# Kernel tuning notes

Measured on AMD Instinct MI355X. Metric: run time of the kernel, lower is better.

The kernel has to match this reference:

```python
import jax, jax.numpy as jnp
import numpy as np

N = 100_000      # nodes
M = 200_000      # hyperedges
E = 1_000_000    # incidence pairs
D_IN = 64
HEADS, D_OUT = 8, 16   # linear out = 8*16 = 128


def setup_inputs() -> dict:
    key = jax.random.key(0)
    k = jax.random.split(key, 7)
    X = jax.random.normal(k[0], (N, D_IN), dtype=jnp.float32)
    vertex = jax.random.randint(k[1], (E,), 0, N, dtype=jnp.int32)
    edges = jax.random.randint(k[2], (E,), 0, M, dtype=jnp.int32)
    dege = jax.random.uniform(k[3], (M, 1), dtype=jnp.float32)
    degv = jax.random.uniform(k[4], (N, 1), dtype=jnp.float32)
    W = jax.random.normal(k[5], (D_IN, HEADS * D_OUT), dtype=jnp.float32) / np.sqrt(D_IN)
    b = jax.random.normal(k[6], (HEADS * D_OUT,), dtype=jnp.float32) * 0.01
    return {"X": X, "vertex": vertex, "edges": edges, "dege": dege, "degv": degv, "W": W, "b": b}


def reference(X, vertex, edges, dege, degv, W, b):
    n_nodes = X.shape[0]
    n_edges = dege.shape[0]
    # vertex -> hyperedge aggregation (first_aggregate = 'mean')
    Xve = X[vertex]                                               # [E, D]
    sums = jax.ops.segment_sum(Xve, edges, num_segments=n_edges)  # [M, D]
    counts = jax.ops.segment_sum(jnp.ones((edges.shape[0],), X.dtype), edges, num_segments=n_edges)
    Xe = sums / jnp.maximum(counts, 1.0)[:, None]                 # empty edges -> 0
    Xe = Xe * dege
    # hyperedge -> vertex aggregation (sum)
    Xev = Xe[edges]                                               # [E, D]
    Xv = jax.ops.segment_sum(Xev, vertex, num_segments=n_nodes)   # [N, D]
    Xv = Xv * degv
    # normalize_l2: row norm is computed on a DETACHED tensor in torch
    rownorm = jnp.linalg.norm(jax.lax.stop_gradient(Xv), axis=1, keepdims=True)
    scale = jnp.where(rownorm > 0, 1.0 / rownorm, 0.0)
    Xn = Xv * scale
    return Xn @ W + b
```

## Files before the change

kernel.cpp:

```cpp
#include <hip/hip_runtime.h>


#define DIN 64
#define DOUT 128
#define CH 4096
#define BSHIFT 10
#define PAYBITS 18
#define PAYMASK ((1u << PAYBITS) - 1u)

typedef float f32x4 __attribute__((ext_vector_type(4)));
typedef short bf16x8 __attribute__((ext_vector_type(8)));

__device__ __forceinline__ unsigned short f2b(float f) {
  unsigned u = __float_as_uint(f);
  u = u + 0x7fffu + ((u >> 16) & 1u);
  return (unsigned short)(u >> 16);
}
__device__ __forceinline__ float b2f(unsigned s) {
  return __uint_as_float(s << 16);
}

__global__ __launch_bounds__(256) void p1_hist(
    const int* __restrict__ vertex, const int* __restrict__ edges,
    int* __restrict__ G, int E, int BKE, int BK, int NCH) {
  __shared__ int h[512];
  for (int i = threadIdx.x; i < BK; i += 256) h[i] = 0;
  __syncthreads();
  int c = blockIdx.x;
  int s = c * CH, e_ = min(E, s + CH);
  for (int i = s + threadIdx.x; i < e_; i += 256) {
    atomicAdd(&h[edges[i] >> BSHIFT], 1);
    atomicAdd(&h[BKE + (vertex[i] >> BSHIFT)], 1);
  }
  __syncthreads();
  for (int b = threadIdx.x; b < BK; b += 256) G[(size_t)b * NCH + c] = h[b];
}

__global__ __launch_bounds__(256) void p1b_rowscan(
    int* __restrict__ G, int* __restrict__ rowTot, int NCH) {
  int b = blockIdx.x;
  int* row = G + (size_t)b * NCH;
  __shared__ int wsum[4];
  __shared__ int carry;
  if (threadIdx.x == 0) carry = 0;
  __syncthreads();
  for (int base = 0; base < NCH; base += 256) {
    int i = base + threadIdx.x;
    int v = (i < NCH) ? row[i] : 0;
    int lane = threadIdx.x & 63, wid = threadIdx.x >> 6;
    int inc = v;
    #pragma unroll
    for (int o = 1; o < 64; o <<= 1) {
      int t = __shfl_up(inc, o);
      if (lane >= o) inc += t;
    }
    if (lane == 63) wsum[wid] = inc;
    __syncthreads();
    int woff = carry;
    for (int w = 0; w < wid; ++w) woff += wsum[w];
    int excl = woff + inc - v;
    if (i < NCH) row[i] = excl;
    __syncthreads();
    if (threadIdx.x == 0) carry += wsum[0] + wsum[1] + wsum[2] + wsum[3];
    __syncthreads();
  }
  if (threadIdx.x == 0) rowTot[b] = carry;
}

__global__ void p1c_scan(const int* __restrict__ rowTot,
                         int* __restrict__ bucketBase, int BK) {
  if (threadIdx.x == 0 && blockIdx.x == 0) {
    int s = 0;
    for (int b = 0; b < BK; ++b) { bucketBase[b] = s; s += rowTot[b]; }
    bucketBase[BK] = s;
  }
}

__global__ __launch_bounds__(256) void p2_scatter(
    const int* __restrict__ vertex, const int* __restrict__ edges,
    const int* __restrict__ G, const int* __restrict__ bucketBase,
    unsigned* __restrict__ temp, int E, int BKE, int BK, int NCH) {
  __shared__ int curs[512];
  int c = blockIdx.x;
  for (int b = threadIdx.x; b < BK; b += 256)
    curs[b] = bucketBase[b] + G[(size_t)b * NCH + c];
  __syncthreads();
  int s = c * CH, e_ = min(E, s + CH);
  for (int i = s + threadIdx.x; i < e_; i += 256) {
    int e = edges[i], v = vertex[i];
    int pE = atomicAdd(&curs[e >> BSHIFT], 1);
    temp[pE] = ((unsigned)(e & 1023) << PAYBITS) | (unsigned)v;
    int pV = atomicAdd(&curs[BKE + (v >> BSHIFT)], 1);
    temp[pV] = ((unsigned)(v & 1023) << PAYBITS) | (unsigned)e;
  }
}

__global__ __launch_bounds__(256) void p3_sort(
    const unsigned* __restrict__ temp, const int* __restrict__ bucketBase,
    int* __restrict__ off, int* __restrict__ perm, int BKE, int M, int N) {
  __shared__ int hist[1024];
  __shared__ int pos[1024];
  __shared__ int wsum[4];
  int g = blockIdx.x;
  bool isE = g < BKE;
  int gg = isE ? g : g - BKE;
  int keyBase = gg << BSHIFT;
  int cap = isE ? M : N;
  int offBase = (isE ? 0 : M) + keyBase;
  int fineCount = min(1024, cap - keyBase);
  int pairBase = bucketBase[g], pairEnd = bucketBase[g + 1];
  int cnt = pairEnd - pairBase;

  for (int i = threadIdx.x; i < 1024; i += 256) hist[i] = 0;
  __syncthreads();
  for (int i = threadIdx.x; i < cnt; i += 256)
    atomicAdd(&hist[temp[pairBase + i] >> PAYBITS], 1);
  __syncthreads();

  int t4 = threadIdx.x * 4;
  int a0 = hist[t4], a1 = hist[t4 + 1], a2 = hist[t4 + 2], a3 = hist[t4 + 3];
  int tsum = a0 + a1 + a2 + a3;
  int lane = threadIdx.x & 63, wid = threadIdx.x >> 6;
  int inc = tsum;
  #pragma unroll
  for (int o = 1; o < 64; o <<= 1) {
    int t = __shfl_up(inc, o);
    if (lane >= o) inc += t;
  }
  if (lane == 63) wsum[wid] = inc;
  __syncthreads();
  int woff = 0;
  for (int w = 0; w < wid; ++w) woff += wsum[w];
  int excl = woff + inc - tsum;
  pos[t4] = excl; pos[t4 + 1] = excl + a0;
  pos[t4 + 2] = excl + a0 + a1; pos[t4 + 3] = excl + a0 + a1 + a2;
  __syncthreads();

  for (int f = threadIdx.x; f < fineCount; f += 256)
    off[offBase + f] = pairBase + pos[f] + hist[f];
  for (int f = threadIdx.x; f < 1024; f += 256) pos[f] += pairBase;
  __syncthreads();

  for (int i = threadIdx.x; i < cnt; i += 256) {
    unsigned p = temp[pairBase + i];
    int q = atomicAdd(&pos[p >> PAYBITS], 1);
    perm[q] = (int)(p & PAYMASK);
  }
}


__global__ __launch_bounds__(256) void k_xcast(
    const float* __restrict__ X, unsigned short* __restrict__ Xb, int total4) {
  int i = blockIdx.x * 256 + threadIdx.x;
  if (i >= total4) return;
  float4 a = ((const float4*)X)[i];
  ushort4 r;
  r.x = f2b(a.x); r.y = f2b(a.y); r.z = f2b(a.z); r.w = f2b(a.w);
  ((ushort4*)Xb)[i] = r;
}

__global__ __launch_bounds__(256) void k_edge(
    const unsigned short* __restrict__ Xb, const int* __restrict__ off,
    const int* __restrict__ perm, const float* __restrict__ dege,
    unsigned short* __restrict__ Xe, int M) {
  long long gid = (long long)blockIdx.x * 256 + threadIdx.x;
  int wv = (int)(gid >> 6);
  int lane = threadIdx.x & 63;
  int g = lane >> 4, li = lane & 15;
  int e = wv * 4 + g;
  bool valid = e < M;
  int start = 0, end = 0;
  if (valid) { start = e ? off[e - 1] : 0; end = off[e]; }
  int deg = end - start;
  int myidx = (valid && li < deg) ? perm[start + li] : 0;
  int jmax = min(deg, 16);
  int jw = jmax;
  jw = max(jw, __shfl_xor(jw, 16));
  jw = max(jw, __shfl_xor(jw, 32));
  const uint2* X2 = (const uint2*)Xb;
  float4 acc = make_float4(0.f, 0.f, 0.f, 0.f);
  #pragma unroll 4
  for (int j = 0; j < jw; ++j) {
    int v0 = __shfl(myidx, (g << 4) + j);
    if (j < jmax) {
      uint2 a = X2[(size_t)v0 * 16 + li];
      acc.x += b2f(a.x & 0xffffu); acc.y += b2f(a.x >> 16);
      acc.z += b2f(a.y & 0xffffu); acc.w += b2f(a.y >> 16);
    }
  }
  for (int j = 16; j < deg; ++j) {
    int v0 = perm[start + j];
    uint2 a = X2[(size_t)v0 * 16 + li];
    acc.x += b2f(a.x & 0xffffu); acc.y += b2f(a.x >> 16);
    acc.z += b2f(a.y & 0xffffu); acc.w += b2f(a.y >> 16);
  }
  if (valid) {
    float s = dege[e] / fmaxf((float)deg, 1.0f);
    ushort4 r;
    r.x = f2b(acc.x * s); r.y = f2b(acc.y * s);
    r.z = f2b(acc.z * s); r.w = f2b(acc.w * s);
    ((ushort4*)Xe)[(size_t)e * 16 + li] = r;
  }
}

__global__ __launch_bounds__(256) void k_nodeagg(
    const unsigned short* __restrict__ Xe, const int* __restrict__ off,
    const int* __restrict__ perm, const float* __restrict__ degv,
    unsigned short* __restrict__ xn, int N, int M) {
  long long gid = (long long)blockIdx.x * 256 + threadIdx.x;
  int wv = (int)(gid >> 6);
  int lane = threadIdx.x & 63;
  int g = lane >> 4, li = lane & 15;
  int node = wv * 4 + g;
  bool valid = node < N;
  int start = 0, end = 0;
  if (valid) { start = off[M + node - 1]; end = off[M + node]; }
  int deg = end - start;
  int myidx = (valid && li < deg) ? perm[start + li] : 0;
  int jmax = min(deg, 16);
  int jw = jmax;
  jw = max(jw, __shfl_xor(jw, 16));
  jw = max(jw, __shfl_xor(jw, 32));
  const uint2* Xe2 = (const uint2*)Xe;
  float4 acc = make_float4(0.f, 0.f, 0.f, 0.f);
  #pragma unroll 4
  for (int j = 0; j < jw; ++j) {
    int e0 = __shfl(myidx, (g << 4) + j);
    if (j < jmax) {
      uint2 a = Xe2[(size_t)e0 * 16 + li];
      acc.x += b2f(a.x & 0xffffu); acc.y += b2f(a.x >> 16);
      acc.z += b2f(a.y & 0xffffu); acc.w += b2f(a.y >> 16);
    }
  }
  for (int j = 16; j < deg; ++j) {
    int e0 = perm[start + j];
    uint2 a = Xe2[(size_t)e0 * 16 + li];
    acc.x += b2f(a.x & 0xffffu); acc.y += b2f(a.x >> 16);
    acc.z += b2f(a.y & 0xffffu); acc.w += b2f(a.y >> 16);
  }
  float dv = valid ? degv[node] : 0.f;
  acc.x *= dv; acc.y *= dv; acc.z *= dv; acc.w *= dv;
  float ss = acc.x * acc.x + acc.y * acc.y + acc.z * acc.z + acc.w * acc.w;
  #pragma unroll
  for (int o = 1; o <= 8; o <<= 1) ss += __shfl_xor(ss, o);
  float sc = ss > 0.0f ? 1.0f / sqrtf(ss) : 0.0f;
  if (valid) {
    ushort4 r;
    r.x = f2b(acc.x * sc); r.y = f2b(acc.y * sc);
    r.z = f2b(acc.z * sc); r.w = f2b(acc.w * sc);
    ((ushort4*)xn)[(size_t)node * 16 + li] = r;
  }
}

#define WPAD 72
__global__ __launch_bounds__(256) void k_linear(
    const unsigned short* __restrict__ xn, const float* __restrict__ W,
    const float* __restrict__ bias, float* __restrict__ out, int N) {
  __shared__ unsigned short Wt[DOUT * WPAD];
  for (int i = threadIdx.x; i < DIN * DOUT; i += 256) {
    int k = i >> 7, c = i & 127;
    Wt[c * WPAD + k] = f2b(W[i]);
  }
  __syncthreads();
  int lane = threadIdx.x & 63;
  int wid = threadIdx.x >> 6;
  int r = lane & 15, h = lane >> 4;

  bf16x8 Bf[8][2];
  #pragma unroll
  for (int c = 0; c < 8; ++c) {
    #pragma unroll
    for (int ks = 0; ks < 2; ++ks) {
      int col = c * 16 + r;
      int k0 = ks * 32 + h * 8;
      Bf[c][ks] = *(const bf16x8*)&Wt[col * WPAD + k0];
    }
  }
  float bcol[8];
  #pragma unroll
  for (int c = 0; c < 8; ++c) bcol[c] = bias[c * 16 + r];

  int strips = (N + 15) >> 4;
  for (int s = blockIdx.x * 4 + wid; s < strips; s += gridDim.x * 4) {
    int row0 = s << 4;
    const unsigned short* xrow = xn + (size_t)(row0 + r) * DIN;
    bf16x8 a0 = *(const bf16x8*)&xrow[h * 8];
    bf16x8 a1 = *(const bf16x8*)&xrow[32 + h * 8];
    #pragma unroll
    for (int c = 0; c < 8; ++c) {
      f32x4 acc = {bcol[c], bcol[c], bcol[c], bcol[c]};
      acc = __builtin_amdgcn_mfma_f32_16x16x32_bf16(a0, Bf[c][0], acc, 0, 0, 0);
      acc = __builtin_amdgcn_mfma_f32_16x16x32_bf16(a1, Bf[c][1], acc, 0, 0, 0);
      #pragma unroll
      for (int q = 0; q < 4; ++q)
        out[(size_t)(row0 + h * 4 + q) * DOUT + c * 16 + r] = acc[q];
    }
  }
}

extern "C" void kernel_launch(void* const* d_in, const int* in_sizes, int n_in,
                              void* d_out, int out_size, void* d_ws, size_t ws_size,
                              hipStream_t stream) {
  const float* X      = (const float*)d_in[0];
  const int*   vertex = (const int*)d_in[1];
  const int*   edges  = (const int*)d_in[2];
  const float* dege   = (const float*)d_in[3];
  const float* degv   = (const float*)d_in[4];
  const float* W      = (const float*)d_in[5];
  const float* b      = (const float*)d_in[6];
  float* out = (float*)d_out;

  int N = in_sizes[0] / DIN;
  int E = in_sizes[1];
  int M = in_sizes[3];

  int NCH = (E + CH - 1) / CH;
  int BKE = (M + 1023) >> BSHIFT;
  int BKV = (N + 1023) >> BSHIFT;
  int BK  = BKE + BKV;

  unsigned short* Xe = (unsigned short*)d_ws;
  unsigned short* Xb = Xe + (size_t)M * DIN;
  int*   off  = (int*)(Xb + (size_t)N * DIN);
  int*   perm = off + (M + N);
  char*  R    = (char*)(perm + 2 * (size_t)E);
  unsigned*       temp = (unsigned*)R;
  unsigned short* xn   = (unsigned short*)R;
  size_t rBytes = (size_t)2 * E * 4;
  size_t xBytes = (size_t)N * DIN * 2;
  char*  R2   = R + (rBytes > xBytes ? rBytes : xBytes);
  int*   G    = (int*)R2;
  int*   rowTot = G + (size_t)BK * NCH;
  int*   bucketBase = rowTot + BK;

  int xcast4 = N * DIN / 4;
  k_xcast<<<(xcast4 + 255) / 256, 256, 0, stream>>>(X, Xb, xcast4);

  p1_hist<<<NCH, 256, 0, stream>>>(vertex, edges, G, E, BKE, BK, NCH);
  p1b_rowscan<<<BK, 256, 0, stream>>>(G, rowTot, NCH);
  p1c_scan<<<1, 64, 0, stream>>>(rowTot, bucketBase, BK);
  p2_scatter<<<NCH, 256, 0, stream>>>(vertex, edges, G, bucketBase, temp, E, BKE, BK, NCH);
  p3_sort<<<BK, 256, 0, stream>>>(temp, bucketBase, off, perm, BKE, M, N);

  int edgeBlocks = (M + 15) / 16;
  k_edge<<<edgeBlocks, 256, 0, stream>>>(Xb, off, perm, dege, Xe, M);

  int nodeBlocks = (N + 15) / 16;
  k_nodeagg<<<nodeBlocks, 256, 0, stream>>>(Xe, off, perm, degv, xn, N, M);

  k_linear<<<1024, 256, 0, stream>>>(xn, W, b, out, N);
}
```

Baseline: 159.6 us.

## Fuse xcast into histogram, merge bucket scan via last-block, halve bucket size

The bf16 cast of X now runs in extra blocks of the histogram kernel, and the single-thread bucket prefix scan is folded into the row-scan kernel through a last-block-done atomic counter. Together these remove two kernel launches and the serial one-thread scan. The coarse bucket width drops from 1024 to 512 keys, which doubles the number of sort blocks and gives p3_sort more parallelism, at the cost of larger shared histograms in p1 and p2. The k_linear grid is now sized from the row count instead of being fixed at 1024 blocks.

```diff
diff --git a/kernel.cpp b/kernel.cpp
--- a/kernel.cpp
+++ b/kernel.cpp
@@ -4,9 +4,11 @@
 #define DIN 64
 #define DOUT 128
 #define CH 4096
-#define BSHIFT 10
+#define BSHIFT 9
+#define FINE 512
 #define PAYBITS 18
 #define PAYMASK ((1u << PAYBITS) - 1u)
+#define XB 256
 
 typedef float f32x4 __attribute__((ext_vector_type(4)));
 typedef short bf16x8 __attribute__((ext_vector_type(8)));
@@ -20,10 +22,23 @@
   return __uint_as_float(s << 16);
 }
 
-__global__ __launch_bounds__(256) void p1_hist(
+__global__ __launch_bounds__(256) void k_p1(
     const int* __restrict__ vertex, const int* __restrict__ edges,
-    int* __restrict__ G, int E, int BKE, int BK, int NCH) {
-  __shared__ int h[512];
+    int* __restrict__ G, const float* __restrict__ X,
+    unsigned short* __restrict__ Xb, int* __restrict__ done,
+    int E, int BKE, int BK, int NCH, int total4) {
+  if (blockIdx.x == 0 && threadIdx.x == 0) *done = 0;
+  if (blockIdx.x >= (unsigned)NCH) {
+    int xb = blockIdx.x - NCH;
+    for (int i = xb * 256 + threadIdx.x; i < total4; i += XB * 256) {
+      float4 a = ((const float4*)X)[i];
+      ushort4 r;
+      r.x = f2b(a.x); r.y = f2b(a.y); r.z = f2b(a.z); r.w = f2b(a.w);
+      ((ushort4*)Xb)[i] = r;
+    }
+    return;
+  }
+  __shared__ int h[1024];
   for (int i = threadIdx.x; i < BK; i += 256) h[i] = 0;
   __syncthreads();
   int c = blockIdx.x;
@@ -36,12 +51,14 @@
   for (int b = threadIdx.x; b < BK; b += 256) G[(size_t)b * NCH + c] = h[b];
 }
 
-__global__ __launch_bounds__(256) void p1b_rowscan(
-    int* __restrict__ G, int* __restrict__ rowTot, int NCH) {
+__global__ __launch_bounds__(256) void k_p1b(
+    int* __restrict__ G, int* __restrict__ rowTot, int* __restrict__ bucketBase,
+    int* __restrict__ done, int NCH, int BK) {
   int b = blockIdx.x;
   int* row = G + (size_t)b * NCH;
   __shared__ int wsum[4];
   __shared__ int carry;
+  __shared__ bool amLast;
   if (threadIdx.x == 0) carry = 0;
   __syncthreads();
   for (int base = 0; base < NCH; base += 256) {
@@ -64,23 +81,44 @@
     if (threadIdx.x == 0) carry += wsum[0] + wsum[1] + wsum[2] + wsum[3];
     __syncthreads();
   }
-  if (threadIdx.x == 0) rowTot[b] = carry;
-}
-
-__global__ void p1c_scan(const int* __restrict__ rowTot,
-                         int* __restrict__ bucketBase, int BK) {
-  if (threadIdx.x == 0 && blockIdx.x == 0) {
-    int s = 0;
-    for (int b = 0; b < BK; ++b) { bucketBase[b] = s; s += rowTot[b]; }
-    bucketBase[BK] = s;
-  }
+  if (threadIdx.x == 0) {
+    rowTot[b] = carry;
+    __threadfence();
+    amLast = (atomicAdd(done, 1) == gridDim.x - 1);
+  }
+  __syncthreads();
+  if (!amLast) return;
+
+  if (threadIdx.x == 0) carry = 0;
+  __syncthreads();
+  for (int base = 0; base < BK; base += 256) {
+    int i = base + threadIdx.x;
+    int v = (i < BK) ? atomicAdd(&rowTot[i], 0) : 0;
+    int lane = threadIdx.x & 63, wid = threadIdx.x >> 6;
+    int inc = v;
+    #pragma unroll
+    for (int o = 1; o < 64; o <<= 1) {
+      int t = __shfl_up(inc, o);
+      if (lane >= o) inc += t;
+    }
+    if (lane == 63) wsum[wid] = inc;
+    __syncthreads();
+    int woff = carry;
+    for (int w = 0; w < wid; ++w) woff += wsum[w];
+    int excl = woff + inc - v;
+    if (i < BK) bucketBase[i] = excl;
+    __syncthreads();
+    if (threadIdx.x == 0) carry += wsum[0] + wsum[1] + wsum[2] + wsum[3];
+    __syncthreads();
+  }
+  if (threadIdx.x == 0) bucketBase[BK] = carry;
 }
 
 __global__ __launch_bounds__(256) void p2_scatter(
     const int* __restrict__ vertex, const int* __restrict__ edges,
     const int* __restrict__ G, const int* __restrict__ bucketBase,
     unsigned* __restrict__ temp, int E, int BKE, int BK, int NCH) {
-  __shared__ int curs[512];
+  __shared__ int curs[1024];
   int c = blockIdx.x;
   for (int b = threadIdx.x; b < BK; b += 256)
     curs[b] = bucketBase[b] + G[(size_t)b * NCH + c];
@@ -89,17 +127,17 @@
   for (int i = s + threadIdx.x; i < e_; i += 256) {
     int e = edges[i], v = vertex[i];
     int pE = atomicAdd(&curs[e >> BSHIFT], 1);
-    temp[pE] = ((unsigned)(e & 1023) << PAYBITS) | (unsigned)v;
+    temp[pE] = ((unsigned)(e & (FINE - 1)) << PAYBITS) | (unsigned)v;
     int pV = atomicAdd(&curs[BKE + (v >> BSHIFT)], 1);
-    temp[pV] = ((unsigned)(v & 1023) << PAYBITS) | (unsigned)e;
+    temp[pV] = ((unsigned)(v & (FINE - 1)) << PAYBITS) | (unsigned)e;
   }
 }
 
 __global__ __launch_bounds__(256) void p3_sort(
     const unsigned* __restrict__ temp, const int* __restrict__ bucketBase,
     int* __restrict__ off, int* __restrict__ perm, int BKE, int M, int N) {
-  __shared__ int hist[1024];
-  __shared__ int pos[1024];
+  __shared__ int hist[FINE];
+  __shared__ int pos[FINE];
   __shared__ int wsum[4];
   int g = blockIdx.x;
   bool isE = g < BKE;
@@ -107,19 +145,19 @@
   int keyBase = gg << BSHIFT;
   int cap = isE ? M : N;
   int offBase = (isE ? 0 : M) + keyBase;
-  int fineCount = min(1024, cap - keyBase);
+  int fineCount = min(FINE, cap - keyBase);
   int pairBase = bucketBase[g], pairEnd = bucketBase[g + 1];
   int cnt = pairEnd - pairBase;
 
-  for (int i = threadIdx.x; i < 1024; i += 256) hist[i] = 0;
+  for (int i = threadIdx.x; i < FINE; i += 256) hist[i] = 0;
   __syncthreads();
   for (int i = threadIdx.x; i < cnt; i += 256)
     atomicAdd(&hist[temp[pairBase + i] >> PAYBITS], 1);
   __syncthreads();
 
-  int t4 = threadIdx.x * 4;
-  int a0 = hist[t4], a1 = hist[t4 + 1], a2 = hist[t4 + 2], a3 = hist[t4 + 3];
-  int tsum = a0 + a1 + a2 + a3;
+  int t2 = threadIdx.x * 2;
+  int a0 = hist[t2], a1 = hist[t2 + 1];
+  int tsum = a0 + a1;
   int lane = threadIdx.x & 63, wid = threadIdx.x >> 6;
   int inc = tsum;
   #pragma unroll
@@ -132,13 +170,12 @@
   int woff = 0;
   for (int w = 0; w < wid; ++w) woff += wsum[w];
   int excl = woff + inc - tsum;
-  pos[t4] = excl; pos[t4 + 1] = excl + a0;
-  pos[t4 + 2] = excl + a0 + a1; pos[t4 + 3] = excl + a0 + a1 + a2;
+  pos[t2] = excl; pos[t2 + 1] = excl + a0;
   __syncthreads();
 
   for (int f = threadIdx.x; f < fineCount; f += 256)
     off[offBase + f] = pairBase + pos[f] + hist[f];
-  for (int f = threadIdx.x; f < 1024; f += 256) pos[f] += pairBase;
+  for (int f = threadIdx.x; f < FINE; f += 256) pos[f] += pairBase;
   __syncthreads();
 
   for (int i = threadIdx.x; i < cnt; i += 256) {
@@ -148,16 +185,6 @@
   }
 }
 
-
-__global__ __launch_bounds__(256) void k_xcast(
-    const float* __restrict__ X, unsigned short* __restrict__ Xb, int total4) {
-  int i = blockIdx.x * 256 + threadIdx.x;
-  if (i >= total4) return;
-  float4 a = ((const float4*)X)[i];
-  ushort4 r;
-  r.x = f2b(a.x); r.y = f2b(a.y); r.z = f2b(a.z); r.w = f2b(a.w);
-  ((ushort4*)Xb)[i] = r;
-}
 
 __global__ __launch_bounds__(256) void k_edge(
     const unsigned short* __restrict__ Xb, const int* __restrict__ off,
@@ -315,8 +342,8 @@
   int M = in_sizes[3];
 
   int NCH = (E + CH - 1) / CH;
-  int BKE = (M + 1023) >> BSHIFT;
-  int BKV = (N + 1023) >> BSHIFT;
+  int BKE = (M + FINE - 1) >> BSHIFT;
+  int BKV = (N + FINE - 1) >> BSHIFT;
   int BK  = BKE + BKV;
 
   unsigned short* Xe = (unsigned short*)d_ws;
@@ -332,14 +359,14 @@
   int*   G    = (int*)R2;
   int*   rowTot = G + (size_t)BK * NCH;
   int*   bucketBase = rowTot + BK;
-
-  int xcast4 = N * DIN / 4;
-  k_xcast<<<(xcast4 + 255) / 256, 256, 0, stream>>>(X, Xb, xcast4);
-
-  p1_hist<<<NCH, 256, 0, stream>>>(vertex, edges, G, E, BKE, BK, NCH);
-  p1b_rowscan<<<BK, 256, 0, stream>>>(G, rowTot, NCH);
-  p1c_scan<<<1, 64, 0, stream>>>(rowTot, bucketBase, BK);
-  p2_scatter<<<NCH, 256, 0, stream>>>(vertex, edges, G, bucketBase, temp, E, BKE, BK, NCH);
+  int*   done = bucketBase + BK + 1;
+
+  int total4 = N * DIN / 4;
+  k_p1<<<NCH + XB, 256, 0, stream>>>(vertex, edges, G, X, Xb, done,
+                                     E, BKE, BK, NCH, total4);
+  k_p1b<<<BK, 256, 0, stream>>>(G, rowTot, bucketBase, done, NCH, BK);
+  p2_scatter<<<NCH, 256, 0, stream>>>(vertex, edges, G, bucketBase, temp,
+                                      E, BKE, BK, NCH);
   p3_sort<<<BK, 256, 0, stream>>>(temp, bucketBase, off, perm, BKE, M, N);
 
   int edgeBlocks = (M + 15) / 16;
@@ -348,5 +375,7 @@
   int nodeBlocks = (N + 15) / 16;
   k_nodeagg<<<nodeBlocks, 256, 0, stream>>>(Xe, off, perm, degv, xn, N, M);
 
-  k_linear<<<1024, 256, 0, stream>>>(xn, W, b, out, N);
-}
+  int strips = (N + 15) >> 4;
+  int linBlocks = (strips + 3) / 4;
+  k_linear<<<linBlocks, 256, 0, stream>>>(xn, W, b, out, N);
+}
```

After: 147.4 us. 7.6% less time.
